# Optimization experiments

Measured on AMD Instinct MI355X. Metric: run time of the kernel, lower is better.

The kernel has to match this reference:

```python
import jax, jax.numpy as jnp
import numpy as np
import math

SEQ, BATCH, H, E, V = 2048, 64, 512, 256, 50257


def _gru_cell(x, h, W_ih, W_hh, b_ih, b_hh):
    # PyTorch GRU cell: gates ordered (r, z, n)
    gi = x @ W_ih.T + b_ih            # [B, 3H]
    gh = h @ W_hh.T + b_hh            # [B, 3H]
    i_r, i_z, i_n = jnp.split(gi, 3, axis=1)
    h_r, h_z, h_n = jnp.split(gh, 3, axis=1)
    r = jax.nn.sigmoid(i_r + h_r)
    z = jax.nn.sigmoid(i_z + h_z)
    n = jnp.tanh(i_n + r * h_n)
    return (1.0 - z) * n + z * h


def setup_inputs() -> dict:
    key = jax.random.key(0)
    ks = jax.random.split(key, 14)
    s = 1.0 / math.sqrt(H)
    inp = {
        "inputs": jax.random.randint(ks[0], (BATCH,), 0, V),
        "dec_hidden": jax.random.normal(ks[1], (2, BATCH, H), jnp.float32),
        "enc_outputs": jax.random.normal(ks[2], (SEQ, BATCH, H), jnp.float32),
        "emb": jax.random.normal(ks[3], (V, E), jnp.float32),
        # layer 0: input dim = H + E
        "W_ih0": jax.random.uniform(ks[4], (3 * H, H + E), jnp.float32, -s, s),
        "W_hh0": jax.random.uniform(ks[5], (3 * H, H), jnp.float32, -s, s),
        "b_ih0": jax.random.uniform(ks[6], (3 * H,), jnp.float32, -s, s),
        "b_hh0": jax.random.uniform(ks[7], (3 * H,), jnp.float32, -s, s),
        # layer 1: input dim = H
        "W_ih1": jax.random.uniform(ks[8], (3 * H, H), jnp.float32, -s, s),
        "W_hh1": jax.random.uniform(ks[9], (3 * H, H), jnp.float32, -s, s),
        "b_ih1": jax.random.uniform(ks[10], (3 * H,), jnp.float32, -s, s),
        "b_hh1": jax.random.uniform(ks[11], (3 * H,), jnp.float32, -s, s),
        "out_W": jax.random.uniform(ks[12], (V, H), jnp.float32, -s, s),
        "out_b": jax.random.uniform(ks[13], (V,), jnp.float32, -s, s),
    }
    return inp


def reference(inputs, dec_hidden, enc_outputs, emb,
              W_ih0, W_hh0, b_ih0, b_hh0,
              W_ih1, W_hh1, b_ih1, b_hh1,
              out_W, out_b):
    # --- dot-product attention (vectorized over seq) ---
    h_top = dec_hidden[-1]                                     # [B, H]
    scale = 1.0 / math.sqrt(H)
    energy = jnp.einsum('bh,sbh->sb', h_top, enc_outputs) * scale  # [S, B]
    alpha = jax.nn.softmax(energy, axis=0)                     # softmax over seq
    context = jnp.einsum('sb,sbh->bh', alpha, enc_outputs)     # [B, H]
    # --- embed + concat ---
    embeddings = emb[inputs]                                   # [B, E]
    x = jnp.concatenate([embeddings, context], axis=1)         # [B, E+H]
    # --- 2-layer GRU, single time step (eval mode: no dropout) ---
    h0 = _gru_cell(x, dec_hidden[0], W_ih0, W_hh0, b_ih0, b_hh0)
    h1 = _gru_cell(h0, dec_hidden[1], W_ih1, W_hh1, b_ih1, b_hh1)
    new_hidden = jnp.stack([h0, h1], axis=0)                   # [2, B, H]
    # --- vocab projection ---
    logits = h1 @ out_W.T + out_b                              # [B, V]
    return logits, new_hidden
```

## Files before the change

kernel.cpp:

```cpp
#include <hip/hip_runtime.h>
#include <math.h>

#define SEQ   2048
#define BATCH 64
#define HDIM  512
#define EDIM  256
#define VOCAB 50257
#define BH    (BATCH * HDIM)
#define G3    (3 * HDIM)
#define NCOL  (2 * G3)

typedef __attribute__((ext_vector_type(4))) float f32x4;
typedef __attribute__((ext_vector_type(8))) short bf16x8;

__device__ __forceinline__ unsigned short f2bf(float x) {
    unsigned int u = __float_as_uint(x);
    u += 0x7fffu + ((u >> 16) & 1u);
    return (unsigned short)(u >> 16);
}

__device__ __forceinline__ bf16x8 pack8(float4 a, float4 b) {
    bf16x8 r;
    r[0] = (short)f2bf(a.x); r[1] = (short)f2bf(a.y);
    r[2] = (short)f2bf(a.z); r[3] = (short)f2bf(a.w);
    r[4] = (short)f2bf(b.x); r[5] = (short)f2bf(b.y);
    r[6] = (short)f2bf(b.z); r[7] = (short)f2bf(b.w);
    return r;
}

__device__ __forceinline__ bf16x8 cvt8(const float* p) {
    return pack8(*(const float4*)p, *(const float4*)(p + 4));
}

__global__ __launch_bounds__(256)
void attn_partial(const float* __restrict__ enc, const float* __restrict__ dec,
                  float* __restrict__ pm, float* __restrict__ pl,
                  float* __restrict__ pacc, int P, int rows) {
    const int lane = threadIdx.x & 63;
    const int wave = threadIdx.x >> 6;
    const int p = blockIdx.x * 4 + wave;
    const int b = blockIdx.y;
    const int s0 = p * rows;
    const float scale = 0.044194173824159216f;

    const float4* qp = (const float4*)(dec + BH + (size_t)b * HDIM + 8 * lane);
    float4 q0 = qp[0], q1 = qp[1];
    float qa[8] = {q0.x, q0.y, q0.z, q0.w, q1.x, q1.y, q1.z, q1.w};

    float m = -INFINITY, l = 0.f;
    float acc[8] = {0.f, 0.f, 0.f, 0.f, 0.f, 0.f, 0.f, 0.f};

    #pragma unroll 2
    for (int r = 0; r < rows; r += 4) {
        float va[4][8];
        #pragma unroll
        for (int j = 0; j < 4; ++j) {
            const float4* vp = (const float4*)(enc +
                ((size_t)(s0 + r + j) * BATCH + b) * HDIM + 8 * lane);
            float4 t0 = vp[0], t1 = vp[1];
            va[j][0] = t0.x; va[j][1] = t0.y; va[j][2] = t0.z; va[j][3] = t0.w;
            va[j][4] = t1.x; va[j][5] = t1.y; va[j][6] = t1.z; va[j][7] = t1.w;
        }
        float e[4];
        #pragma unroll
        for (int j = 0; j < 4; ++j) {
            float d = 0.f;
            #pragma unroll
            for (int i = 0; i < 8; ++i) d = fmaf(va[j][i], qa[i], d);
            e[j] = d;
        }
        #pragma unroll
        for (int off = 32; off > 0; off >>= 1) {
            #pragma unroll
            for (int j = 0; j < 4; ++j) e[j] += __shfl_xor(e[j], off, 64);
        }
        #pragma unroll
        for (int j = 0; j < 4; ++j) e[j] *= scale;
        float m4 = fmaxf(fmaxf(e[0], e[1]), fmaxf(e[2], e[3]));
        float em = fmaxf(m, m4);
        float f  = __expf(m - em);
        float w0 = __expf(e[0] - em), w1 = __expf(e[1] - em);
        float w2 = __expf(e[2] - em), w3 = __expf(e[3] - em);
        l = l * f + (w0 + w1 + w2 + w3);
        #pragma unroll
        for (int i = 0; i < 8; ++i) {
            float a = acc[i] * f;
            a = fmaf(w0, va[0][i], a);
            a = fmaf(w1, va[1][i], a);
            a = fmaf(w2, va[2][i], a);
            acc[i] = fmaf(w3, va[3][i], a);
        }
        m = em;
    }

    float* pa = pacc + ((size_t)b * P + p) * HDIM + 8 * lane;
    #pragma unroll
    for (int i = 0; i < 8; ++i) pa[i] = acc[i];
    if (lane == 0) { pm[b * P + p] = m; pl[b * P + p] = l; }
}

__global__ __launch_bounds__(512)
void attn_combine(const float* __restrict__ pm, const float* __restrict__ pl,
                  const float* __restrict__ pacc, const float* __restrict__ dec,
                  const float* __restrict__ emb, const int* __restrict__ inputs,
                  unsigned short* __restrict__ xbf,
                  unsigned short* __restrict__ d0bf,
                  unsigned short* __restrict__ d1bf, int P) {
    __shared__ float s_coef[128];
    __shared__ float s_inv;
    const int b = blockIdx.x;
    const int t = threadIdx.x;

    if (t < 64) {
        float mloc = -INFINITY;
        for (int p = t; p < P; p += 64) mloc = fmaxf(mloc, pm[b * P + p]);
        #pragma unroll
        for (int off = 32; off > 0; off >>= 1) mloc = fmaxf(mloc, __shfl_xor(mloc, off, 64));
        float d = 0.f;
        for (int p = t; p < P; p += 64) {
            float c = __expf(pm[b * P + p] - mloc);
            s_coef[p] = c;
            d = fmaf(c, pl[b * P + p], d);
        }
        #pragma unroll
        for (int off = 32; off > 0; off >>= 1) d += __shfl_xor(d, off, 64);
        if (t == 0) s_inv = 1.f / d;
    }
    __syncthreads();

    float c = 0.f;
    const float* pa = pacc + (size_t)b * P * HDIM + t;
    #pragma unroll 4
    for (int p = 0; p < P; ++p) c = fmaf(s_coef[p], pa[(size_t)p * HDIM], c);
    float ctx = c * s_inv;

    xbf[(size_t)b * (EDIM + HDIM) + EDIM + t] = f2bf(ctx);
    if (t < EDIM)
        xbf[(size_t)b * (EDIM + HDIM) + t] = f2bf(emb[(size_t)inputs[b] * EDIM + t]);
    d0bf[(size_t)b * HDIM + t] = f2bf(dec[(size_t)b * HDIM + t]);
    d1bf[(size_t)b * HDIM + t] = f2bf(dec[BH + (size_t)b * HDIM + t]);
}

template<int K1>
__global__ __launch_bounds__(256)
void gru_gemm(const unsigned short* __restrict__ Aih,
              const unsigned short* __restrict__ Ahh,
              const float* __restrict__ Wih,
              const float* __restrict__ Whh,
              float* __restrict__ part) {
    const int lane = threadIdx.x & 63;
    const int nt = blockIdx.x * 4 + (threadIdx.x >> 6);
    const int kc = blockIdx.y;
    const int nn = lane & 15;
    const int koff = (lane >> 4) * 8;

    const bool ih = nt < 96;
    const int col16 = ih ? nt : nt - 96;
    const int g = col16 * 16 + nn;
    const int K = ih ? K1 : HDIM;
    const int kchunk = K >> 1;
    const int k0 = kc * kchunk;

    const float* wrow = (ih ? Wih : Whh) + (size_t)g * K + k0 + koff;
    const unsigned short* arow = (ih ? Aih : Ahh) + (size_t)nn * K + k0 + koff;

    f32x4 acc[4];
    #pragma unroll
    for (int mt = 0; mt < 4; ++mt) acc[mt] = (f32x4){0, 0, 0, 0};

    const int nks = kchunk >> 5;
    #pragma unroll 4
    for (int ks = 0; ks < nks; ++ks) {
        bf16x8 bf = cvt8(wrow + 32 * ks);
        #pragma unroll
        for (int mt = 0; mt < 4; ++mt) {
            bf16x8 a = *(const bf16x8*)(arow + (size_t)mt * 16 * K + 32 * ks);
            acc[mt] = __builtin_amdgcn_mfma_f32_16x16x32_bf16(a, bf, acc[mt], 0, 0, 0);
        }
    }

    const int col = col16 * 16 + nn + (ih ? 0 : G3);
    float* pp = part + ((size_t)kc * NCOL + col) * 64 + (lane >> 4) * 4;
    #pragma unroll
    for (int mt = 0; mt < 4; ++mt)
        *(f32x4*)(pp + mt * 16) = acc[mt];
}

__global__ __launch_bounds__(256)
void gru_gate(const float* __restrict__ part,
              const float* __restrict__ hprev,
              const float* __restrict__ bih, const float* __restrict__ bhh,
              float* __restrict__ hout, unsigned short* __restrict__ houtBf) {
    const int gidx = blockIdx.x * 256 + threadIdx.x;
    const int b = gidx & 63;
    const int h = gidx >> 6;

    #define PRD(c) (part[(size_t)(c) * 64 + b] + part[(size_t)((c) + NCOL) * 64 + b])
    float ir = PRD(h),            hr = PRD(G3 + h);
    float iz = PRD(HDIM + h),     hz = PRD(G3 + HDIM + h);
    float in_ = PRD(2 * HDIM + h), hn = PRD(G3 + 2 * HDIM + h);
    #undef PRD

    float r = 1.f / (1.f + __expf(-(ir + bih[h] + hr + bhh[h])));
    float z = 1.f / (1.f + __expf(-(iz + bih[HDIM + h] + hz + bhh[HDIM + h])));
    float n = tanhf(in_ + bih[2 * HDIM + h] + r * (hn + bhh[2 * HDIM + h]));
    float hp = hprev[(size_t)b * HDIM + h];
    float hnew = (1.f - z) * n + z * hp;

    hout[(size_t)b * HDIM + h] = hnew;
    houtBf[(size_t)b * HDIM + h] = f2bf(hnew);
}

__global__ __launch_bounds__(256)
void vocab_proj_mfma(const unsigned short* __restrict__ h1bf,
                     const float* __restrict__ Wout,
                     const float* __restrict__ bout,
                     float* __restrict__ logits) {
    const int NPAIR = (VOCAB + 31) / 32;
    const int lane = threadIdx.x & 63;
    const int w = blockIdx.x * 4 + (threadIdx.x >> 6);
    if (w >= NPAIR) return;

    const int nn = lane & 15;
    const int koff = (lane >> 4) * 8;
    const int vA = w * 32 + nn;
    const int vB = vA + 16;
    const int vAc = min(vA, VOCAB - 1);
    const int vBc = min(vB, VOCAB - 1);

    const float* wrowA = Wout + (size_t)vAc * HDIM + koff;
    const float* wrowB = Wout + (size_t)vBc * HDIM + koff;
    const unsigned short* arow = h1bf + nn * HDIM + koff;

    f32x4 accA[4], accB[4];
    #pragma unroll
    for (int mt = 0; mt < 4; ++mt) { accA[mt] = (f32x4){0,0,0,0}; accB[mt] = (f32x4){0,0,0,0}; }

    float4 pa0 = *(const float4*)(wrowA);
    float4 pa1 = *(const float4*)(wrowA + 4);
    float4 pb0 = *(const float4*)(wrowB);
    float4 pb1 = *(const float4*)(wrowB + 4);

    #pragma unroll
    for (int ks = 0; ks < 16; ++ks) {
        float4 ca0 = pa0, ca1 = pa1, cb0 = pb0, cb1 = pb1;
        if (ks < 15) {
            pa0 = *(const float4*)(wrowA + 32 * (ks + 1));
            pa1 = *(const float4*)(wrowA + 32 * (ks + 1) + 4);
            pb0 = *(const float4*)(wrowB + 32 * (ks + 1));
            pb1 = *(const float4*)(wrowB + 32 * (ks + 1) + 4);
        }
        bf16x8 bA = pack8(ca0, ca1);
        bf16x8 bB = pack8(cb0, cb1);
        #pragma unroll
        for (int mt = 0; mt < 4; ++mt) {
            bf16x8 a = *(const bf16x8*)(arow + (size_t)mt * 16 * HDIM + 32 * ks);
            accA[mt] = __builtin_amdgcn_mfma_f32_16x16x32_bf16(a, bA, accA[mt], 0, 0, 0);
            accB[mt] = __builtin_amdgcn_mfma_f32_16x16x32_bf16(a, bB, accB[mt], 0, 0, 0);
        }
    }

    const int b0 = (lane >> 4) * 4;
    if (vA < VOCAB) {
        const float bias = bout[vA];
        #pragma unroll
        for (int mt = 0; mt < 4; ++mt)
            #pragma unroll
            for (int r = 0; r < 4; ++r)
                logits[(size_t)(mt * 16 + b0 + r) * VOCAB + vA] = accA[mt][r] + bias;
    }
    if (vB < VOCAB) {
        const float bias = bout[vB];
        #pragma unroll
        for (int mt = 0; mt < 4; ++mt)
            #pragma unroll
            for (int r = 0; r < 4; ++r)
                logits[(size_t)(mt * 16 + b0 + r) * VOCAB + vB] = accB[mt][r] + bias;
    }
}

extern "C" void kernel_launch(void* const* d_in, const int* in_sizes, int n_in,
                              void* d_out, int out_size, void* d_ws, size_t ws_size,
                              hipStream_t stream) {
    const int*   inputs = (const int*)d_in[0];
    const float* dec    = (const float*)d_in[1];
    const float* enc    = (const float*)d_in[2];
    const float* emb    = (const float*)d_in[3];
    const float* Wih0   = (const float*)d_in[4];
    const float* Whh0   = (const float*)d_in[5];
    const float* bih0   = (const float*)d_in[6];
    const float* bhh0   = (const float*)d_in[7];
    const float* Wih1   = (const float*)d_in[8];
    const float* Whh1   = (const float*)d_in[9];
    const float* bih1   = (const float*)d_in[10];
    const float* bhh1   = (const float*)d_in[11];
    const float* Wout   = (const float*)d_in[12];
    const float* bout   = (const float*)d_in[13];
    float* out = (float*)d_out;

    int P = 128;
    while (P > 4) {
        size_t need = ((size_t)P * BATCH * (HDIM + 2) + 2u * NCOL * 64) * sizeof(float)
                      + 2u * (BATCH * (EDIM + HDIM) + 4u * BH);
        if (need <= ws_size) break;
        P >>= 1;
    }
    const int rows = SEQ / P;

    float* w    = (float*)d_ws;
    float* pm   = w;
    float* pl   = pm + (size_t)P * BATCH;
    float* pacc = pl + (size_t)P * BATCH;
    float* part = pacc + (size_t)P * BATCH * HDIM;
    unsigned short* xbf  = (unsigned short*)(part + 2 * (size_t)NCOL * 64);
    unsigned short* d0bf = xbf + (size_t)BATCH * (EDIM + HDIM);
    unsigned short* d1bf = d0bf + BH;
    unsigned short* h0bf = d1bf + BH;
    unsigned short* h1bf = h0bf + BH;

    float* h0out = out + (size_t)BATCH * VOCAB;
    float* h1out = h0out + BH;

    attn_partial<<<dim3(P / 4, BATCH), 256, 0, stream>>>(enc, dec, pm, pl, pacc, P, rows);
    attn_combine<<<BATCH, 512, 0, stream>>>(pm, pl, pacc, dec, emb, inputs, xbf, d0bf, d1bf, P);

    gru_gemm<EDIM + HDIM><<<dim3(48, 2), 256, 0, stream>>>(xbf, d0bf, Wih0, Whh0, part);
    gru_gate<<<128, 256, 0, stream>>>(part, dec, bih0, bhh0, h0out, h0bf);
    gru_gemm<HDIM><<<dim3(48, 2), 256, 0, stream>>>(h0bf, d1bf, Wih1, Whh1, part);
    gru_gate<<<128, 256, 0, stream>>>(part, dec + BH, bih1, bhh1, h1out, h1bf);

    const int NPAIR = (VOCAB + 31) / 32;
    vocab_proj_mfma<<<(NPAIR + 3) / 4, 256, 0, stream>>>(h1bf, Wout, bout, out);
}
```

Before: 142.8 us.

## Stage vocab projection weights through LDS with async double-buffered global_load_lds

Rewrites the vocab projection so that each 256-thread block handles 64 vocab rows. The fp32 out_W tiles are streamed into LDS in 128-column chunks using global_load_lds DMA with double buffering and an XOR swizzle to avoid bank conflicts. The goal is fully coalesced, asynchronous weight loads that overlap with MFMA work, replacing the strided per-lane register loads. It adds LDS usage and per-chunk barriers, and halves the vocab columns per wave, which could reduce MFMA density.

```diff
diff --git a/kernel.cpp b/kernel.cpp
--- a/kernel.cpp
+++ b/kernel.cpp
@@ -1,5 +1,6 @@
 #include <hip/hip_runtime.h>
 #include <math.h>
+#include <stdint.h>
 
 #define SEQ   2048
 #define BATCH 64
@@ -30,6 +31,14 @@
 
 __device__ __forceinline__ bf16x8 cvt8(const float* p) {
     return pack8(*(const float4*)p, *(const float4*)(p + 4));
+}
+
+__device__ __forceinline__ void gload_lds16(const float* g, float* l) {
+    auto gp = reinterpret_cast<const __attribute__((address_space(1))) uint32_t*>(
+        reinterpret_cast<uintptr_t>(g));
+    auto lp = reinterpret_cast<__attribute__((address_space(3))) uint32_t*>(
+        reinterpret_cast<uintptr_t>(l));
+    __builtin_amdgcn_global_load_lds(gp, lp, 16, 0, 0);
 }
 
 __global__ __launch_bounds__(256)
@@ -211,71 +220,77 @@
     houtBf[(size_t)b * HDIM + h] = f2bf(hnew);
 }
 
+#define VB   64
+#define BKC  128
+#define NCHK (HDIM / BKC)
+
 __global__ __launch_bounds__(256)
-void vocab_proj_mfma(const unsigned short* __restrict__ h1bf,
-                     const float* __restrict__ Wout,
-                     const float* __restrict__ bout,
-                     float* __restrict__ logits) {
-    const int NPAIR = (VOCAB + 31) / 32;
-    const int lane = threadIdx.x & 63;
-    const int w = blockIdx.x * 4 + (threadIdx.x >> 6);
-    if (w >= NPAIR) return;
+void vocab_proj_lds(const unsigned short* __restrict__ h1bf,
+                    const float* __restrict__ Wout,
+                    const float* __restrict__ bout,
+                    float* __restrict__ logits) {
+    __shared__ float lds[2][VB * BKC];
+    const int t = threadIdx.x;
+    const int lane = t & 63;
+    const int wv = t >> 6;
+    const int v0 = blockIdx.x * VB;
+
+    const float* gsrc[8];
+    #pragma unroll
+    for (int i = 0; i < 8; ++i) {
+        int q = (wv * 8 + i) * 64 + lane;
+        int r = q >> 5, g = q & 31;
+        int rc = min(v0 + r, VOCAB - 1);
+        gsrc[i] = Wout + (size_t)rc * HDIM + ((g ^ (r & 7)) << 2);
+    }
 
     const int nn = lane & 15;
-    const int koff = (lane >> 4) * 8;
-    const int vA = w * 32 + nn;
-    const int vB = vA + 16;
-    const int vAc = min(vA, VOCAB - 1);
-    const int vBc = min(vB, VOCAB - 1);
-
-    const float* wrowA = Wout + (size_t)vAc * HDIM + koff;
-    const float* wrowB = Wout + (size_t)vBc * HDIM + koff;
-    const unsigned short* arow = h1bf + nn * HDIM + koff;
-
-    f32x4 accA[4], accB[4];
-    #pragma unroll
-    for (int mt = 0; mt < 4; ++mt) { accA[mt] = (f32x4){0,0,0,0}; accB[mt] = (f32x4){0,0,0,0}; }
-
-    float4 pa0 = *(const float4*)(wrowA);
-    float4 pa1 = *(const float4*)(wrowA + 4);
-    float4 pb0 = *(const float4*)(wrowB);
-    float4 pb1 = *(const float4*)(wrowB + 4);
-
-    #pragma unroll
-    for (int ks = 0; ks < 16; ++ks) {
-        float4 ca0 = pa0, ca1 = pa1, cb0 = pb0, cb1 = pb1;
-        if (ks < 15) {
-            pa0 = *(const float4*)(wrowA + 32 * (ks + 1));
-            pa1 = *(const float4*)(wrowA + 32 * (ks + 1) + 4);
-            pb0 = *(const float4*)(wrowB + 32 * (ks + 1));
-            pb1 = *(const float4*)(wrowB + 32 * (ks + 1) + 4);
-        }
-        bf16x8 bA = pack8(ca0, ca1);
-        bf16x8 bB = pack8(cb0, cb1);
-        #pragma unroll
-        for (int mt = 0; mt < 4; ++mt) {
-            bf16x8 a = *(const bf16x8*)(arow + (size_t)mt * 16 * HDIM + 32 * ks);
-            accA[mt] = __builtin_amdgcn_mfma_f32_16x16x32_bf16(a, bA, accA[mt], 0, 0, 0);
-            accB[mt] = __builtin_amdgcn_mfma_f32_16x16x32_bf16(a, bB, accB[mt], 0, 0, 0);
-        }
-    }
-
-    const int b0 = (lane >> 4) * 4;
-    if (vA < VOCAB) {
-        const float bias = bout[vA];
+    const int koff16 = lane >> 4;
+    const int rloc = wv * 16 + nn;
+    const int swz = rloc & 7;
+    const unsigned short* arow = h1bf + (size_t)nn * HDIM + koff16 * 8;
+
+    f32x4 acc[4];
+    #pragma unroll
+    for (int mt = 0; mt < 4; ++mt) acc[mt] = (f32x4){0, 0, 0, 0};
+
+    #pragma unroll
+    for (int i = 0; i < 8; ++i)
+        gload_lds16(gsrc[i], &lds[0][(wv * 8 + i) * 256]);
+    __syncthreads();
+
+    for (int c = 0; c < NCHK; ++c) {
+        const int cur = c & 1;
+        if (c + 1 < NCHK) {
+            #pragma unroll
+            for (int i = 0; i < 8; ++i)
+                gload_lds16(gsrc[i] + (c + 1) * BKC, &lds[cur ^ 1][(wv * 8 + i) * 256]);
+        }
+        #pragma unroll
+        for (int ksl = 0; ksl < 4; ++ksl) {
+            const int ga = ksl * 8 + koff16 * 2;
+            const float4 w0 = *(const float4*)&lds[cur][(rloc * 32 + (ga ^ swz)) * 4];
+            const float4 w1 = *(const float4*)&lds[cur][(rloc * 32 + ((ga + 1) ^ swz)) * 4];
+            bf16x8 bfrag = pack8(w0, w1);
+            const int ksg = c * 4 + ksl;
+            #pragma unroll
+            for (int mt = 0; mt < 4; ++mt) {
+                bf16x8 a = *(const bf16x8*)(arow + (size_t)mt * 16 * HDIM + 32 * ksg);
+                acc[mt] = __builtin_amdgcn_mfma_f32_16x16x32_bf16(a, bfrag, acc[mt], 0, 0, 0);
+            }
+        }
+        __syncthreads();
+    }
+
+    const int v = v0 + rloc;
+    if (v < VOCAB) {
+        const float bias = bout[v];
+        const int b0 = koff16 * 4;
         #pragma unroll
         for (int mt = 0; mt < 4; ++mt)
             #pragma unroll
             for (int r = 0; r < 4; ++r)
-                logits[(size_t)(mt * 16 + b0 + r) * VOCAB + vA] = accA[mt][r] + bias;
-    }
-    if (vB < VOCAB) {
-        const float bias = bout[vB];
-        #pragma unroll
-        for (int mt = 0; mt < 4; ++mt)
-            #pragma unroll
-            for (int r = 0; r < 4; ++r)
-                logits[(size_t)(mt * 16 + b0 + r) * VOCAB + vB] = accB[mt][r] + bias;
+                logits[(size_t)(mt * 16 + b0 + r) * VOCAB + v] = acc[mt][r] + bias;
     }
 }
 
@@ -329,6 +344,6 @@
     gru_gemm<HDIM><<<dim3(48, 2), 256, 0, stream>>>(h0bf, d1bf, Wih1, Whh1, part);
     gru_gate<<<128, 256, 0, stream>>>(part, dec + BH, bih1, bhh1, h1out, h1bf);
 
-    const int NPAIR = (VOCAB + 31) / 32;
-    vocab_proj_mfma<<<(NPAIR + 3) / 4, 256, 0, stream>>>(h1bf, Wout, bout, out);
-}
+    const int NB = (VOCAB + VB - 1) / VB;
+    vocab_proj_lds<<<NB, 256, 0, stream>>>(h1bf, Wout, bout, out);
+}
```

New measurement: 149.1 us. 1.04x slower.
